# Performance work log

Hardware: AMD Instinct MI355X
Metric: run time of the kernel (lower is better)

Reference implementation:

```python
import jax, jax.numpy as jnp
import numpy as np

G = 8          # groups
EPS = 1e-5     # GroupNorm eps

def maxpool(x, k):
    pad = k // 2
    return jax.lax.reduce_window(x, -jnp.inf, jax.lax.max,
                                 (1, 1, k, k), (1, 1, 1, 1),
                                 [(0, 0), (0, 0), (pad, pad), (pad, pad)])

def conv1x1(x, w):
    # w: [out, in], x: [B, in, H, W]
    return jnp.einsum('oi,bihw->bohw', w, x)

def setup_inputs() -> dict:
    key = jax.random.key(0)
    ks = jax.random.split(key, 8)
    B, Cin, H, W = 16, 256, 64, 64
    planes = 256
    s = 0.05
    return {
        'x': jax.random.normal(ks[0], (B, Cin, H, W), jnp.float32),
        'mask': jax.random.uniform(ks[1], (B, 2, H, W), jnp.float32),
        'Wt': jax.random.normal(ks[2], (planes, Cin), jnp.float32) * s,
        'Wtm': jax.random.normal(ks[3], (1, 2), jnp.float32) * s,
        'Wp': jax.random.normal(ks[4], (planes // 2, Cin), jnp.float32) * s,
        'Wg': jax.random.normal(ks[5], (planes // 2, Cin), jnp.float32) * s,
        'Wz': jax.random.normal(ks[6], (G, Cin // G, planes // G), jnp.float32) * s,
        'gamma': jnp.ones((Cin,), jnp.float32),
        'beta': jnp.zeros((Cin,), jnp.float32),
    }

def reference(x, mask, Wt, Wtm, Wp, Wg, Wz, gamma, beta):
    B, Cin, H, W = x.shape
    planes = Wt.shape[0]
    cg = planes // G
    HW = H * W

    t = conv1x1(x, Wt)                      # [B, planes, H, W]
    t_mask = conv1x1(mask, Wtm)             # [B, 1, H, W]
    t = t * t_mask + t

    p = conv1x1(x, Wp)                      # [B, planes//2, H, W]
    p = jnp.concatenate([p, maxpool(p, 3), maxpool(p, 5)], axis=1)
    g = conv1x1(x, Wg)
    g = jnp.concatenate([g, maxpool(g, 3), maxpool(g, 5)], axis=1)
    # torch.split(_, cg) + loop over `groups` consumes only the first `planes` channels
    p = p[:, :planes]
    g = g[:, :planes]

    # kernel(), vectorized over groups: softmax over spatial, global scalar att per group
    ts = jax.nn.softmax(t.reshape(B, G, cg, HW), axis=-1)        # softmax dim=2 of [b,c,hw]
    pf = p.reshape(B, G, cg * HW)
    gf = g.reshape(B, G, cg * HW)
    att = jnp.einsum('bgn,bgn->bg', pf, gf)                      # bmm([b,1,n],[b,n,1])
    xk = (att[:, :, None, None] * ts).reshape(B, planes, H, W)

    # grouped 1x1 conv z: planes -> inplanes with G groups
    xz = jnp.einsum('goi,bgihw->bgohw', Wz,
                    xk.reshape(B, G, cg, H, W)).reshape(B, Cin, H, W)

    # GroupNorm(G, Cin)
    xg = xz.reshape(B, G, -1)
    mu = xg.mean(-1, keepdims=True)
    var = xg.var(-1, keepdims=True)
    xn = ((xg - mu) * jax.lax.rsqrt(var + EPS)).reshape(B, Cin, H, W)
    xn = xn * gamma[None, :, None, None] + beta[None, :, None, None]

    return xn + x
```

## Files before the change

### kernel.cpp

```cpp
#include <hip/hip_runtime.h>
#include <math.h>

#define B_      16
#define CIN     256
#define HW_     4096
#define PLANES  256
#define G_      8
#define EPSV    1e-5f

typedef unsigned short u16;
typedef __attribute__((ext_vector_type(8))) short short8;
typedef __attribute__((ext_vector_type(4))) float f32x4;

__device__ inline u16 f2bf(float f) {
    union { float f; unsigned u; } v; v.f = f;
    unsigned u = v.u;
    return (u16)((u + 0x7fffu + ((u >> 16) & 1u)) >> 16);
}
__device__ inline float bf2f(u16 h) {
    union { unsigned u; float f; } v; v.u = ((unsigned)h) << 16;
    return v.f;
}

__global__ __launch_bounds__(256) void k_packA(
    const float* __restrict__ Wt, const float* __restrict__ Wp,
    const float* __restrict__ Wg,
    u16* __restrict__ pAhi, u16* __restrict__ pAlo)
{
    int t = blockIdx.x * 256 + threadIdx.x;
    int lane = t & 63;
    int mb   = (t >> 6) & 7;
    int kt   = (t >> 9) & 7;
    int rt   = (t >> 12) & 3;
    int row = rt * 128 + mb * 16 + (lane & 15);
    int k0  = kt * 32 + (lane >> 4) * 8;
    const float* src;
    if      (row < 256) src = Wt + (size_t)row * 256;
    else if (row < 384) src = Wp + (size_t)(row - 256) * 256;
    else                src = Wg + (size_t)(row - 384) * 256;
    u16 hv[8], lv[8];
    #pragma unroll
    for (int j = 0; j < 8; ++j) {
        float w = src[k0 + j];
        u16 h = f2bf(w);
        hv[j] = h;
        lv[j] = f2bf(w - bf2f(h));
    }
    *(short8*)(pAhi + (size_t)t * 8) = *(short8*)hv;
    *(short8*)(pAlo + (size_t)t * 8) = *(short8*)lv;
}

__global__ __launch_bounds__(256) void k_transpose(
    const float* __restrict__ x, u16* __restrict__ xThi,
    u16* __restrict__ xTlo)
{
    __shared__ float tile[32][129];
    int tid = threadIdx.x;
    int px0 = blockIdx.x * 128;
    int c0  = blockIdx.y * 32;
    int bg  = blockIdx.z;

    #pragma unroll
    for (int it = 0; it < 16; ++it) {
        int flat = it * 256 + tid;
        int c_l = flat >> 7, p_l = flat & 127;
        tile[c_l][p_l] = x[((size_t)bg * 256 + c0 + c_l) * 4096 + px0 + p_l];
    }
    __syncthreads();
    #pragma unroll
    for (int it = 0; it < 8; ++it) {
        int flat = it * 256 + tid;
        int p_l = flat >> 4;
        int c_l = (flat & 15) * 2;
        float v0 = tile[c_l][p_l], v1 = tile[c_l + 1][p_l];
        u16 h0 = f2bf(v0), h1 = f2bf(v1);
        u16 l0 = f2bf(v0 - bf2f(h0)), l1 = f2bf(v1 - bf2f(h1));
        size_t o = ((size_t)bg * 4096 + px0 + p_l) * 256 + c0 + c_l;
        u16 ho[2] = { h0, h1 };
        u16 lo[2] = { l0, l1 };
        *(unsigned*)(xThi + o) = *(unsigned*)ho;
        *(unsigned*)(xTlo + o) = *(unsigned*)lo;
    }
}

__global__ __launch_bounds__(256) void k_tmod_zero(
    const float* __restrict__ mask, const float* __restrict__ Wtm,
    float* __restrict__ tmod, float* __restrict__ att, float* __restrict__ stats)
{
    int idx = blockIdx.x * 256 + threadIdx.x;
    float w0 = Wtm[0], w1 = Wtm[1];
    if (idx < B_ * HW_) {
        int b = idx >> 12, pix = idx & 4095;
        const float* mb = mask + (size_t)b * 2 * HW_;
        tmod[idx] = 1.0f + w0 * mb[pix] + w1 * mb[HW_ + pix];
    }
    if (blockIdx.x == 0) {
        if (threadIdx.x < 128) att[threadIdx.x] = 0.0f;
        stats[threadIdx.x] = 0.0f;
    }
}

#define STAGE(SRC)                                                            \
    _Pragma("unroll")                                                         \
    for (int it = 0; it < 16; ++it) {                                         \
        int cidx = it * 256 + tid;                                            \
        int px   = cidx >> 5;                                                 \
        int boff = (cidx & 31) << 4;                                          \
        short8 v = *(const short8*)((SRC) + (size_t)px * 512 + boff);         \
        *(short8*)(Blds + px * 512 + (boff ^ ((px & 7) << 4))) = v;           \
    }

#define MFMA_PASS(ASRC)                                                       \
    _Pragma("unroll")                                                         \
    for (int kt = 0; kt < 8; ++kt) {                                          \
        short8 a[4], bb[4];                                                   \
        _Pragma("unroll")                                                     \
        for (int m = 0; m < 4; ++m)                                           \
            a[m] = *(const short8*)((ASRC) +                                  \
                ((((size_t)(rt * 8 + kt) * 8) + wm * 4 + m) * 64 + lane) * 8);\
        int off = ((kt * 64) + ((lane >> 4) << 4)) ^ ((lane & 7) << 4);       \
        _Pragma("unroll")                                                     \
        for (int n = 0; n < 4; ++n) {                                         \
            int px = wn * 64 + n * 16 + (lane & 15);                          \
            bb[n] = *(const short8*)(Blds + px * 512 + off);                  \
        }                                                                     \
        _Pragma("unroll")                                                     \
        for (int m = 0; m < 4; ++m)                                           \
            _Pragma("unroll")                                                 \
            for (int n = 0; n < 4; ++n)                                       \
                acc[m][n] = __builtin_amdgcn_mfma_f32_16x16x32_bf16(          \
                    a[m], bb[n], acc[m][n], 0, 0, 0);                         \
    }

__global__ __launch_bounds__(256) void k_mm0(
    const u16* __restrict__ xThi, const u16* __restrict__ pAhi,
    const float* __restrict__ tmod, u16* __restrict__ tbuf)
{
    __shared__ short8 BldsV[4096];
    char* Blds = (char*)BldsV;
    int tid = threadIdx.x, lane = tid & 63, wid = tid >> 6;
    int wm = wid >> 1, wn = wid & 1;
    int pix0 = blockIdx.x * 128;
    int rt   = blockIdx.y;
    int bg   = blockIdx.z;

    const char* srcHi = (const char*)(xThi + ((size_t)bg * 4096 + pix0) * 256);

    f32x4 acc[4][4];
    #pragma unroll
    for (int m = 0; m < 4; ++m)
        #pragma unroll
        for (int n = 0; n < 4; ++n) acc[m][n] = (f32x4)0.0f;

    STAGE(srcHi);
    __syncthreads();
    MFMA_PASS(pAhi);

    int colb = pix0 + wn * 64;
    int rowb = rt * 128 + wm * 64;
    float tm[4];
    #pragma unroll
    for (int n = 0; n < 4; ++n) tm[n] = tmod[bg * 4096 + colb + n * 16 + (lane & 15)];
    #pragma unroll
    for (int m = 0; m < 4; ++m)
        #pragma unroll
        for (int n = 0; n < 4; ++n)
            #pragma unroll
            for (int r = 0; r < 4; ++r) {
                int row = rowb + m * 16 + (lane >> 4) * 4 + r;
                int col = colb + n * 16 + (lane & 15);
                tbuf[((size_t)bg * 256 + row) * 4096 + col] = f2bf(acc[m][n][r] * tm[n]);
            }
}

__global__ __launch_bounds__(256) void k_mm1(
    const u16* __restrict__ xThi, const u16* __restrict__ xTlo,
    const u16* __restrict__ pAhi, const u16* __restrict__ pAlo,
    float* __restrict__ pbuf, float* __restrict__ gbuf)
{
    __shared__ short8 BldsV[4096];
    char* Blds = (char*)BldsV;
    int tid = threadIdx.x, lane = tid & 63, wid = tid >> 6;
    int wm = wid >> 1, wn = wid & 1;
    int pix0 = blockIdx.x * 128;
    int by   = blockIdx.y;
    int rt   = 2 + by;
    int bg   = blockIdx.z;

    const char* srcHi = (const char*)(xThi + ((size_t)bg * 4096 + pix0) * 256);
    const char* srcLo = (const char*)(xTlo + ((size_t)bg * 4096 + pix0) * 256);

    f32x4 acc[4][4];
    #pragma unroll
    for (int m = 0; m < 4; ++m)
        #pragma unroll
        for (int n = 0; n < 4; ++n) acc[m][n] = (f32x4)0.0f;

    STAGE(srcHi);
    __syncthreads();
    MFMA_PASS(pAhi);
    MFMA_PASS(pAlo);
    __syncthreads();
    STAGE(srcLo);
    __syncthreads();
    MFMA_PASS(pAhi);

    float* dst = (by == 0) ? pbuf : gbuf;
    int colb = pix0 + wn * 64;
    int rowb = wm * 64;
    #pragma unroll
    for (int m = 0; m < 4; ++m)
        #pragma unroll
        for (int n = 0; n < 4; ++n)
            #pragma unroll
            for (int r = 0; r < 4; ++r) {
                int row = rowb + m * 16 + (lane >> 4) * 4 + r;
                int col = colb + n * 16 + (lane & 15);
                dst[((size_t)bg * 128 + row) * 4096 + col] = acc[m][n][r];
            }
}

__global__ __launch_bounds__(256) void k_att(
    const float* __restrict__ pbuf, const float* __restrict__ gbuf,
    float* __restrict__ att)
{
    __shared__ float plds[HW_];
    __shared__ float glds[HW_];
    __shared__ float scr[8];
    int c  = blockIdx.x;
    int gi = blockIdx.y;
    int b  = blockIdx.z;
    int tid = threadIdx.x;

    const float* pp = pbuf + ((size_t)b * 128 + gi * 32 + c) * HW_;
    const float* gg = gbuf + ((size_t)b * 128 + gi * 32 + c) * HW_;

    float racc = 0.0f;
    #pragma unroll
    for (int it = 0; it < 4; ++it) {
        int i = it * 1024 + tid * 4;
        float4 pv = *(const float4*)(pp + i);
        float4 gv = *(const float4*)(gg + i);
        *(float4*)(&plds[i]) = pv;
        *(float4*)(&glds[i]) = gv;
        racc += pv.x * gv.x + pv.y * gv.y + pv.z * gv.z + pv.w * gv.w;
    }
    __syncthreads();

    float pacc = 0.0f;
    #pragma unroll 4
    for (int i = tid; i < HW_; i += 256) {
        int h = i >> 6, w = i & 63;
        int h0 = max(h - 1, 0), h1 = min(h + 1, 63);
        int w0 = max(w - 1, 0), w1 = min(w + 1, 63);
        float mp = -3.0e38f, mg = -3.0e38f;
        for (int hh = h0; hh <= h1; ++hh)
            for (int ww = w0; ww <= w1; ++ww) {
                mp = fmaxf(mp, plds[hh * 64 + ww]);
                mg = fmaxf(mg, glds[hh * 64 + ww]);
            }
        pacc += mp * mg;
    }

    #pragma unroll
    for (int off = 32; off > 0; off >>= 1) {
        racc += __shfl_down(racc, off, 64);
        pacc += __shfl_down(pacc, off, 64);
    }
    int lane = tid & 63, wid = tid >> 6;
    if (lane == 0) { scr[wid] = racc; scr[4 + wid] = pacc; }
    __syncthreads();
    if (tid == 0) {
        atomicAdd(&att[b * 8 + gi],     scr[0] + scr[1] + scr[2] + scr[3]);
        atomicAdd(&att[b * 8 + gi + 4], scr[4] + scr[5] + scr[6] + scr[7]);
    }
}

__global__ __launch_bounds__(256) void k_smax(
    const u16* __restrict__ tbuf, float2* __restrict__ rowstat)
{
    __shared__ float scr[8];
    int r = blockIdx.x;
    const u16* tr = tbuf + (size_t)r * HW_;
    int tid = threadIdx.x;
    int lane = tid & 63, wid = tid >> 6;

    float vals[16];
    float mx = -3.0e38f;
    #pragma unroll
    for (int it = 0; it < 2; ++it) {
        short8 v = *(const short8*)(tr + it * 2048 + tid * 8);
        #pragma unroll
        for (int j = 0; j < 8; ++j) {
            float f = bf2f((u16)v[j]);
            vals[it * 8 + j] = f;
            mx = fmaxf(mx, f);
        }
    }
    #pragma unroll
    for (int off = 32; off > 0; off >>= 1) mx = fmaxf(mx, __shfl_down(mx, off, 64));
    if (lane == 0) scr[wid] = mx;
    __syncthreads();
    if (tid == 0) scr[0] = fmaxf(fmaxf(scr[0], scr[1]), fmaxf(scr[2], scr[3]));
    __syncthreads();
    float m = scr[0];
    __syncthreads();

    float s = 0.0f;
    #pragma unroll
    for (int j = 0; j < 16; ++j) s += __expf(vals[j] - m);
    #pragma unroll
    for (int off = 32; off > 0; off >>= 1) s += __shfl_down(s, off, 64);
    if (lane == 0) scr[4 + wid] = s;
    __syncthreads();
    if (tid == 0) {
        float S = scr[4] + scr[5] + scr[6] + scr[7];
        rowstat[r] = make_float2(m, 1.0f / S);
    }
}

__global__ __launch_bounds__(256) void k_xz2(
    u16* __restrict__ tbuf, const float* __restrict__ Wz,
    const float2* __restrict__ rowstat, const float* __restrict__ att,
    float* __restrict__ stats)
{
    __shared__ float wz[32][32];
    __shared__ float2 rs[32];
    __shared__ float scr[8];
    int pt  = blockIdx.x;
    int gi  = blockIdx.y;
    int b   = blockIdx.z;
    int tid = threadIdx.x;
    int px  = pt * 512 + tid * 2;

    const float* wzg = Wz + gi * 1024;
    #pragma unroll
    for (int i = 0; i < 4; ++i) {
        int idx = tid + i * 256;
        wz[idx >> 5][idx & 31] = wzg[idx];
    }
    if (tid < 32) rs[tid] = rowstat[b * 256 + gi * 32 + tid];
    __syncthreads();

    u16* base = tbuf + ((size_t)b * 256 + gi * 32) * HW_;
    float2 v[32];
    #pragma unroll
    for (int i = 0; i < 32; ++i) {
        unsigned rv = *(const unsigned*)(base + (size_t)i * HW_ + px);
        float m = rs[i].x, inv = rs[i].y;
        v[i].x = __expf(bf2f((u16)(rv & 0xffffu)) - m) * inv;
        v[i].y = __expf(bf2f((u16)(rv >> 16)) - m) * inv;
    }

    float a = att[b * 8 + gi];
    float s1 = 0.0f, s2 = 0.0f;
    #pragma unroll
    for (int o = 0; o < 32; ++o) {
        const float4* wzo = (const float4*)(&wz[o][0]);
        float ax = 0.0f, ay = 0.0f;
        #pragma unroll
        for (int j = 0; j < 8; ++j) {
            float4 w = wzo[j];
            ax = fmaf(w.x, v[4*j+0].x, ax); ay = fmaf(w.x, v[4*j+0].y, ay);
            ax = fmaf(w.y, v[4*j+1].x, ax); ay = fmaf(w.y, v[4*j+1].y, ay);
            ax = fmaf(w.z, v[4*j+2].x, ax); ay = fmaf(w.z, v[4*j+2].y, ay);
            ax = fmaf(w.w, v[4*j+3].x, ax); ay = fmaf(w.w, v[4*j+3].y, ay);
        }
        ax *= a; ay *= a;
        unsigned ov = (unsigned)f2bf(ax) | ((unsigned)f2bf(ay) << 16);
        *(unsigned*)(base + (size_t)o * HW_ + px) = ov;
        s1 += ax + ay;
        s2 = fmaf(ax, ax, fmaf(ay, ay, s2));
    }

    #pragma unroll
    for (int off = 32; off > 0; off >>= 1) {
        s1 += __shfl_down(s1, off, 64);
        s2 += __shfl_down(s2, off, 64);
    }
    int lane = tid & 63, wid = tid >> 6;
    if (lane == 0) { scr[wid] = s1; scr[4 + wid] = s2; }
    __syncthreads();
    if (tid == 0) {
        atomicAdd(&stats[(b * 8 + gi) * 2 + 0], scr[0] + scr[1] + scr[2] + scr[3]);
        atomicAdd(&stats[(b * 8 + gi) * 2 + 1], scr[4] + scr[5] + scr[6] + scr[7]);
    }
}

__global__ __launch_bounds__(256) void k_finalize(
    const u16* __restrict__ xzbuf, const float* __restrict__ x,
    const float* __restrict__ stats, const float* __restrict__ gamma,
    const float* __restrict__ beta, float* __restrict__ out)
{
    size_t i0 = ((size_t)blockIdx.x * 256 + threadIdx.x) * 4;
    int c  = (int)((i0 >> 12) & 255);
    int bg = (int)(i0 >> 17);
    float s1 = stats[bg * 2], s2 = stats[bg * 2 + 1];
    const float invN = 1.0f / 131072.0f;
    float mu  = s1 * invN;
    float var = s2 * invN - mu * mu;
    float rs  = rsqrtf(var + EPSV);
    float ga = gamma[c], be = beta[c];

    union { unsigned long long u; u16 h[4]; } vv;
    vv.u = *(const unsigned long long*)(xzbuf + i0);
    float4 xv = *(const float4*)(x + i0);
    float4 o;
    o.x = (bf2f(vv.h[0]) - mu) * rs * ga + be + xv.x;
    o.y = (bf2f(vv.h[1]) - mu) * rs * ga + be + xv.y;
    o.z = (bf2f(vv.h[2]) - mu) * rs * ga + be + xv.z;
    o.w = (bf2f(vv.h[3]) - mu) * rs * ga + be + xv.w;
    *(float4*)(out + i0) = o;
}

extern "C" void kernel_launch(void* const* d_in, const int* in_sizes, int n_in,
                              void* d_out, int out_size, void* d_ws, size_t ws_size,
                              hipStream_t stream)
{
    const float* x     = (const float*)d_in[0];
    const float* mask  = (const float*)d_in[1];
    const float* Wt    = (const float*)d_in[2];
    const float* Wtm   = (const float*)d_in[3];
    const float* Wp    = (const float*)d_in[4];
    const float* Wg    = (const float*)d_in[5];
    const float* Wz    = (const float*)d_in[6];
    const float* gamma = (const float*)d_in[7];
    const float* beta  = (const float*)d_in[8];
    float* out = (float*)d_out;

    char* ws = (char*)d_ws;
    u16*   tbuf  = (u16*)(ws);
    u16*   xThi  = (u16*)(ws + 33554432);
    u16*   xTlo  = (u16*)(ws + 67108864);
    float* pbuf  = (float*)(ws + 100663296);
    float* gbuf  = (float*)(ws + 167772160);
    u16*   pAhi  = (u16*)(ws + 234881024);
    u16*   pAlo  = (u16*)(ws + 235143168);
    float* tmod  = (float*)(ws + 235405312);
    float* att   = (float*)(ws + 235667456);
    float* stats = att + 128;
    float2* rowstat = (float2*)(ws + 235669504);

    k_packA    <<<64, 256, 0, stream>>>(Wt, Wp, Wg, pAhi, pAlo);
    k_tmod_zero<<<256, 256, 0, stream>>>(mask, Wtm, tmod, att, stats);
    k_transpose<<<dim3(32, 8, 16), 256, 0, stream>>>(x, xThi, xTlo);
    k_mm0      <<<dim3(32, 2, 16), 256, 0, stream>>>(xThi, pAhi, tmod, tbuf);
    k_mm1      <<<dim3(32, 2, 16), 256, 0, stream>>>(xThi, xTlo, pAhi, pAlo, pbuf, gbuf);
    k_att      <<<dim3(32, 4, 16), 256, 0, stream>>>(pbuf, gbuf, att);
    k_smax     <<<4096, 256, 0, stream>>>(tbuf, rowstat);
    k_xz2      <<<dim3(8, 8, 16), 256, 0, stream>>>(tbuf, Wz, rowstat, att, stats);
    k_finalize <<<16384, 256, 0, stream>>>(tbuf, x, stats, gamma, beta, out);
}
```

Before: 216.6 us.

## Retile conv GEMMs to 64-pixel blocks covering all output rows per block

The two MFMA GEMM kernels now use 64-pixel tiles, with each block's four waves covering the full set of output rows (256 for mm0, 2x128 for mm1) instead of a 128x128 tile split across blockIdx.y. Each staged x tile is read from global memory once per block rather than once per row-tile block, halving LDS usage and the redundant x reads. The grid changes from 32x2x16 to 64x16, so the block count is unchanged. In exchange, each wave's A-operand footprint is fixed per row tile, and output stores cover narrower column spans.

```diff
diff --git a/kernel.cpp b/kernel.cpp
--- a/kernel.cpp
+++ b/kernel.cpp
@@ -100,9 +100,9 @@
     }
 }
 
-#define STAGE(SRC)                                                            \
+#define STAGE8(SRC)                                                           \
     _Pragma("unroll")                                                         \
-    for (int it = 0; it < 16; ++it) {                                         \
+    for (int it = 0; it < 8; ++it) {                                          \
         int cidx = it * 256 + tid;                                            \
         int px   = cidx >> 5;                                                 \
         int boff = (cidx & 31) << 4;                                          \
@@ -110,18 +110,18 @@
         *(short8*)(Blds + px * 512 + (boff ^ ((px & 7) << 4))) = v;           \
     }
 
-#define MFMA_PASS(ASRC)                                                       \
+#define MFMA_PASS(ASRC, RT, MBB)                                              \
     _Pragma("unroll")                                                         \
     for (int kt = 0; kt < 8; ++kt) {                                          \
         short8 a[4], bb[4];                                                   \
         _Pragma("unroll")                                                     \
         for (int m = 0; m < 4; ++m)                                           \
             a[m] = *(const short8*)((ASRC) +                                  \
-                ((((size_t)(rt * 8 + kt) * 8) + wm * 4 + m) * 64 + lane) * 8);\
+                ((((size_t)((RT) * 8 + kt) * 8) + (MBB) + m) * 64 + lane) * 8);\
         int off = ((kt * 64) + ((lane >> 4) << 4)) ^ ((lane & 7) << 4);       \
         _Pragma("unroll")                                                     \
         for (int n = 0; n < 4; ++n) {                                         \
-            int px = wn * 64 + n * 16 + (lane & 15);                          \
+            int px = n * 16 + (lane & 15);                                    \
             bb[n] = *(const short8*)(Blds + px * 512 + off);                  \
         }                                                                     \
         _Pragma("unroll")                                                     \
@@ -136,13 +136,13 @@
     const u16* __restrict__ xThi, const u16* __restrict__ pAhi,
     const float* __restrict__ tmod, u16* __restrict__ tbuf)
 {
-    __shared__ short8 BldsV[4096];
+    __shared__ short8 BldsV[2048];
     char* Blds = (char*)BldsV;
     int tid = threadIdx.x, lane = tid & 63, wid = tid >> 6;
-    int wm = wid >> 1, wn = wid & 1;
-    int pix0 = blockIdx.x * 128;
-    int rt   = blockIdx.y;
-    int bg   = blockIdx.z;
+    int rt  = wid >> 1;
+    int mbb = (wid & 1) * 4;
+    int pix0 = blockIdx.x * 64;
+    int bg   = blockIdx.y;
 
     const char* srcHi = (const char*)(xThi + ((size_t)bg * 4096 + pix0) * 256);
 
@@ -152,23 +152,21 @@
         #pragma unroll
         for (int n = 0; n < 4; ++n) acc[m][n] = (f32x4)0.0f;
 
-    STAGE(srcHi);
-    __syncthreads();
-    MFMA_PASS(pAhi);
-
-    int colb = pix0 + wn * 64;
-    int rowb = rt * 128 + wm * 64;
+    STAGE8(srcHi);
+    __syncthreads();
+    MFMA_PASS(pAhi, rt, mbb);
+
     float tm[4];
     #pragma unroll
-    for (int n = 0; n < 4; ++n) tm[n] = tmod[bg * 4096 + colb + n * 16 + (lane & 15)];
+    for (int n = 0; n < 4; ++n) tm[n] = tmod[bg * 4096 + pix0 + n * 16 + (lane & 15)];
     #pragma unroll
     for (int m = 0; m < 4; ++m)
         #pragma unroll
         for (int n = 0; n < 4; ++n)
             #pragma unroll
             for (int r = 0; r < 4; ++r) {
-                int row = rowb + m * 16 + (lane >> 4) * 4 + r;
-                int col = colb + n * 16 + (lane & 15);
+                int row = wid * 64 + m * 16 + (lane >> 4) * 4 + r;
+                int col = pix0 + n * 16 + (lane & 15);
                 tbuf[((size_t)bg * 256 + row) * 4096 + col] = f2bf(acc[m][n][r] * tm[n]);
             }
 }
@@ -178,14 +176,13 @@
     const u16* __restrict__ pAhi, const u16* __restrict__ pAlo,
     float* __restrict__ pbuf, float* __restrict__ gbuf)
 {
-    __shared__ short8 BldsV[4096];
+    __shared__ short8 BldsV[2048];
     char* Blds = (char*)BldsV;
     int tid = threadIdx.x, lane = tid & 63, wid = tid >> 6;
-    int wm = wid >> 1, wn = wid & 1;
-    int pix0 = blockIdx.x * 128;
-    int by   = blockIdx.y;
-    int rt   = 2 + by;
-    int bg   = blockIdx.z;
+    int rt  = 2 + (wid >> 1);
+    int mbb = (wid & 1) * 4;
+    int pix0 = blockIdx.x * 64;
+    int bg   = blockIdx.y;
 
     const char* srcHi = (const char*)(xThi + ((size_t)bg * 4096 + pix0) * 256);
     const char* srcLo = (const char*)(xTlo + ((size_t)bg * 4096 + pix0) * 256);
@@ -196,26 +193,24 @@
         #pragma unroll
         for (int n = 0; n < 4; ++n) acc[m][n] = (f32x4)0.0f;
 
-    STAGE(srcHi);
-    __syncthreads();
-    MFMA_PASS(pAhi);
-    MFMA_PASS(pAlo);
-    __syncthreads();
-    STAGE(srcLo);
-    __syncthreads();
-    MFMA_PASS(pAhi);
-
-    float* dst = (by == 0) ? pbuf : gbuf;
-    int colb = pix0 + wn * 64;
-    int rowb = wm * 64;
+    STAGE8(srcHi);
+    __syncthreads();
+    MFMA_PASS(pAhi, rt, mbb);
+    MFMA_PASS(pAlo, rt, mbb);
+    __syncthreads();
+    STAGE8(srcLo);
+    __syncthreads();
+    MFMA_PASS(pAhi, rt, mbb);
+
+    float* dst = (wid < 2) ? pbuf : gbuf;
     #pragma unroll
     for (int m = 0; m < 4; ++m)
         #pragma unroll
         for (int n = 0; n < 4; ++n)
             #pragma unroll
             for (int r = 0; r < 4; ++r) {
-                int row = rowb + m * 16 + (lane >> 4) * 4 + r;
-                int col = colb + n * 16 + (lane & 15);
+                int row = (wid & 1) * 64 + m * 16 + (lane >> 4) * 4 + r;
+                int col = pix0 + n * 16 + (lane & 15);
                 dst[((size_t)bg * 128 + row) * 4096 + col] = acc[m][n][r];
             }
 }
@@ -444,8 +439,8 @@
     k_packA    <<<64, 256, 0, stream>>>(Wt, Wp, Wg, pAhi, pAlo);
     k_tmod_zero<<<256, 256, 0, stream>>>(mask, Wtm, tmod, att, stats);
     k_transpose<<<dim3(32, 8, 16), 256, 0, stream>>>(x, xThi, xTlo);
-    k_mm0      <<<dim3(32, 2, 16), 256, 0, stream>>>(xThi, pAhi, tmod, tbuf);
-    k_mm1      <<<dim3(32, 2, 16), 256, 0, stream>>>(xThi, xTlo, pAhi, pAlo, pbuf, gbuf);
+    k_mm0      <<<dim3(64, 16), 256, 0, stream>>>(xThi, pAhi, tmod, tbuf);
+    k_mm1      <<<dim3(64, 16), 256, 0, stream>>>(xThi, xTlo, pAhi, pAlo, pbuf, gbuf);
     k_att      <<<dim3(32, 4, 16), 256, 0, stream>>>(pbuf, gbuf, att);
     k_smax     <<<4096, 256, 0, stream>>>(tbuf, rowstat);
     k_xz2      <<<dim3(8, 8, 16), 256, 0, stream>>>(tbuf, Wz, rowstat, att, stats);
```

After: 238.8 us. 1.1x slower.
